# Kernel optimization log

Measured on AMD Instinct MI355X. Metric: run time of the kernel, lower is better.

## Reference

```python
import jax, jax.numpy as jnp
import numpy as np

B = 4096  # batch of 28x28 grayscale images


def setup_inputs() -> dict:
    key = jax.random.key(0)
    k1, k2, k3 = jax.random.split(key, 3)
    x = jax.random.uniform(k1, (B, 28, 28), jnp.float32)
    # 5 trainable rotation angles of the fixed 'RandomLayer' circuit
    rand_params = jax.random.uniform(k2, (5,), jnp.float32, 0.0, 2.0 * np.pi)
    W = jax.random.normal(k3, (10, 4 * 14 * 14), jnp.float32) * 0.02
    b = jnp.zeros((10,), jnp.float32)
    return {"x": x, "rand_params": rand_params, "W": W, "b": b}


def _apply1(state, U, w):
    # state: (N,2,2,2,2) complex; apply 2x2 gate U on wire w
    st = jnp.moveaxis(state, w + 1, -1)
    st = st @ U.T
    return jnp.moveaxis(st, -1, w + 1)


def _apply2(state, U, w1, w2):
    # apply 4x4 gate U on (w1,w2), w1 < w2
    st = jnp.moveaxis(state, (w1 + 1, w2 + 1), (-2, -1))
    shp = st.shape
    st = st.reshape(shp[:-2] + (4,)) @ U.T
    return jnp.moveaxis(st.reshape(shp), (-2, -1), (w1 + 1, w2 + 1))


def _ry(t):
    c = jnp.cos(t / 2).astype(jnp.complex64)
    s = jnp.sin(t / 2).astype(jnp.complex64)
    return jnp.stack([jnp.stack([c, -s]), jnp.stack([s, c])])


def _rx(t):
    c = jnp.cos(t / 2).astype(jnp.complex64)
    s = jnp.sin(t / 2).astype(jnp.complex64)
    return jnp.stack([jnp.stack([c, -1j * s]), jnp.stack([-1j * s, c])])


def _rz(t):
    e = jnp.exp(-0.5j * t).astype(jnp.complex64)
    z = jnp.zeros((), jnp.complex64)
    return jnp.stack([jnp.stack([e, z]), jnp.stack([z, jnp.conj(e)])])


_CNOT = jnp.array([[1, 0, 0, 0], [0, 1, 0, 0], [0, 0, 0, 1], [0, 0, 1, 0]], jnp.complex64)


def _forward(x, rand_params, W, b):
    bsz = x.shape[0]
    # 2x2 patches in row-major (r,c) order; pixel order (r,c),(r,c+1),(r+1,c),(r+1,c+1)
    xp = x.reshape(bsz, 14, 2, 14, 2).transpose(0, 1, 3, 2, 4).reshape(bsz, 196, 4)
    ang = xp.reshape(-1, 4)  # (N,4) angles, N = bsz*196
    c, s = jnp.cos(ang / 2), jnp.sin(ang / 2)
    # Ry(theta_i)|0> on each wire => product state built via einsum
    a = [jnp.stack([c[:, i], s[:, i]], axis=-1) for i in range(4)]
    state = jnp.einsum('na,nb,nc,nd->nabcd', a[0], a[1], a[2], a[3]).astype(jnp.complex64)
    # fixed 8-op 'RandomLayer' circuit
    state = _apply1(state, _ry(rand_params[0]), 0)
    state = _apply1(state, _rx(rand_params[1]), 1)
    state = _apply2(state, _CNOT, 0, 1)
    state = _apply1(state, _rz(rand_params[2]), 2)
    state = _apply1(state, _ry(rand_params[3]), 3)
    state = _apply2(state, _CNOT, 2, 3)
    state = _apply1(state, _rx(rand_params[4]), 0)
    state = _apply2(state, _CNOT, 1, 2)
    # PauliZ expectation per wire
    probs = state.real ** 2 + state.imag ** 2  # (N,2,2,2,2)
    z = jnp.array([1.0, -1.0], jnp.float32)
    ez = [jnp.einsum('nabcd,a->n', probs, z),
          jnp.einsum('nabcd,b->n', probs, z),
          jnp.einsum('nabcd,c->n', probs, z),
          jnp.einsum('nabcd,d->n', probs, z)]
    feats = jnp.stack(ez, axis=-1).reshape(bsz, 196 * 4)
    logits = feats @ W.T + b
    return jax.nn.log_softmax(logits, axis=-1)


def reference(x, rand_params, W, b):
    return _forward(x, rand_params, W, b)
```

## Files before the change

### kernel.cpp

```cpp
#include <hip/hip_runtime.h>
#include <math.h>


#define RY_GATE(bit, c_, s_) do {                                          \
    _Pragma("unroll")                                                      \
    for (int j = 0; j < 8; ++j) {                                          \
        const int lo = ((j >> (bit)) << ((bit) + 1)) | (j & ((1 << (bit)) - 1)); \
        const int hi = lo | (1 << (bit));                                  \
        float u0r = sr[lo], u0i = si[lo], u1r = sr[hi], u1i = si[hi];      \
        sr[lo] = (c_) * u0r - (s_) * u1r; si[lo] = (c_) * u0i - (s_) * u1i; \
        sr[hi] = (s_) * u0r + (c_) * u1r; si[hi] = (s_) * u0i + (c_) * u1i; \
    }                                                                      \
} while (0)

#define RX_GATE(bit, c_, s_) do {                                          \
    _Pragma("unroll")                                                      \
    for (int j = 0; j < 8; ++j) {                                          \
        const int lo = ((j >> (bit)) << ((bit) + 1)) | (j & ((1 << (bit)) - 1)); \
        const int hi = lo | (1 << (bit));                                  \
        float u0r = sr[lo], u0i = si[lo], u1r = sr[hi], u1i = si[hi];      \
        sr[lo] = (c_) * u0r + (s_) * u1i; si[lo] = (c_) * u0i - (s_) * u1r; \
        sr[hi] = (c_) * u1r + (s_) * u0i; si[hi] = (c_) * u1i - (s_) * u0r; \
    }                                                                      \
} while (0)

#define RZ_GATE(bit, c_, s_) do {                                          \
    _Pragma("unroll")                                                      \
    for (int j = 0; j < 8; ++j) {                                          \
        const int lo = ((j >> (bit)) << ((bit) + 1)) | (j & ((1 << (bit)) - 1)); \
        const int hi = lo | (1 << (bit));                                  \
        float r0 = sr[lo], i0 = si[lo], r1 = sr[hi], i1 = si[hi];          \
        sr[lo] = (c_) * r0 + (s_) * i0; si[lo] = (c_) * i0 - (s_) * r0;    \
        sr[hi] = (c_) * r1 - (s_) * i1; si[hi] = (c_) * i1 + (s_) * r1;    \
    }                                                                      \
} while (0)

#define CNOT_GATE(cb, tb) do {                                             \
    _Pragma("unroll")                                                      \
    for (int idx = 0; idx < 16; ++idx) {                                   \
        if (((idx >> (cb)) & 1) && !((idx >> (tb)) & 1)) {                 \
            const int o = idx | (1 << (tb));                               \
            float tr = sr[idx], ti = si[idx];                              \
            sr[idx] = sr[o]; si[idx] = si[o];                              \
            sr[o] = tr;      si[o] = ti;                                   \
        }                                                                  \
    }                                                                      \
} while (0)

__global__ __launch_bounds__(256) void quanv_fused_kernel(
    const float* __restrict__ x,
    const float* __restrict__ rp,
    const float* __restrict__ W,
    const float* __restrict__ bias,
    float* __restrict__ out)
{
    const int img = blockIdx.x;
    const int tid = threadIdx.x;

    float acc[10];
#pragma unroll
    for (int c = 0; c < 10; ++c) acc[c] = 0.0f;

    if (tid < 196) {
        const int pr = tid / 14;
        const int pc = tid - pr * 14;
        const float* px = x + (size_t)img * 784 + (2 * pr) * 28 + 2 * pc;
        const float2 r0 = *(const float2*)(px);
        const float2 r1 = *(const float2*)(px + 28);
        const float ang[4] = { r0.x, r0.y, r1.x, r1.y };

        float ca[4], sa[4];
#pragma unroll
        for (int i = 0; i < 4; ++i) __sincosf(0.5f * ang[i], &sa[i], &ca[i]);

        float sr[16], si[16];
#pragma unroll
        for (int a = 0; a < 2; ++a)
#pragma unroll
            for (int b = 0; b < 2; ++b)
#pragma unroll
                for (int c = 0; c < 2; ++c)
#pragma unroll
                    for (int d = 0; d < 2; ++d) {
                        const int idx = a * 8 + b * 4 + c * 2 + d;
                        sr[idx] = (a ? sa[0] : ca[0]) * (b ? sa[1] : ca[1]) *
                                  (c ? sa[2] : ca[2]) * (d ? sa[3] : ca[3]);
                        si[idx] = 0.0f;
                    }

        float gc[5], gs[5];
#pragma unroll
        for (int i = 0; i < 5; ++i) __sincosf(0.5f * rp[i], &gs[i], &gc[i]);

        RY_GATE(3, gc[0], gs[0]);
        RX_GATE(2, gc[1], gs[1]);
        CNOT_GATE(3, 2);
        RZ_GATE(1, gc[2], gs[2]);
        RY_GATE(0, gc[3], gs[3]);
        CNOT_GATE(1, 0);
        RX_GATE(3, gc[4], gs[4]);
        CNOT_GATE(2, 1);

        float ez0 = 0.f, ez1 = 0.f, ez2 = 0.f, ez3 = 0.f;
#pragma unroll
        for (int idx = 0; idx < 16; ++idx) {
            const float p = sr[idx] * sr[idx] + si[idx] * si[idx];
            ez0 += ((idx >> 3) & 1) ? -p : p;
            ez1 += ((idx >> 2) & 1) ? -p : p;
            ez2 += ((idx >> 1) & 1) ? -p : p;
            ez3 += ((idx >> 0) & 1) ? -p : p;
        }

#pragma unroll
        for (int c = 0; c < 10; ++c) {
            const float4 wv = *(const float4*)(W + c * 784 + tid * 4);
            acc[c] = wv.x * ez0 + wv.y * ez1 + wv.z * ez2 + wv.w * ez3;
        }
    }

#pragma unroll
    for (int c = 0; c < 10; ++c) {
        float v = acc[c];
#pragma unroll
        for (int off = 32; off > 0; off >>= 1) v += __shfl_down(v, off, 64);
        acc[c] = v;
    }

    __shared__ float partial[4][10];
    __shared__ float logits_s[10];
    const int wave = tid >> 6;
    const int lane = tid & 63;
    if (lane == 0) {
#pragma unroll
        for (int c = 0; c < 10; ++c) partial[wave][c] = acc[c];
    }
    __syncthreads();

    if (tid < 10) {
        float l = bias[tid];
#pragma unroll
        for (int w = 0; w < 4; ++w) l += partial[w][tid];
        logits_s[tid] = l;
    }
    __syncthreads();

    if (tid < 10) {
        float m = -INFINITY;
#pragma unroll
        for (int c = 0; c < 10; ++c) m = fmaxf(m, logits_s[c]);
        float sum = 0.0f;
#pragma unroll
        for (int c = 0; c < 10; ++c) sum += __expf(logits_s[c] - m);
        out[(size_t)img * 10 + tid] = logits_s[tid] - m - __logf(sum);
    }
}

extern "C" void kernel_launch(void* const* d_in, const int* in_sizes, int n_in,
                              void* d_out, int out_size, void* d_ws, size_t ws_size,
                              hipStream_t stream) {
    const float* x    = (const float*)d_in[0];
    const float* rp   = (const float*)d_in[1];
    const float* W    = (const float*)d_in[2];
    const float* bias = (const float*)d_in[3];
    float* out = (float*)d_out;

    quanv_fused_kernel<<<4096, 256, 0, stream>>>(x, rp, W, bias, out);
}
```

Baseline: 81.97 us.

## Map one image per wavefront and drop shared-memory block reduction

Each 64-lane wavefront now handles a whole image, looping over its 196 patches in four strided passes, so four images share a 256-thread block and the grid shrinks by a factor of four. The final reduction uses xor shuffles within the wave and computes log-softmax in registers, which removes both __syncthreads and the shared-memory partials. The simulation also skips work on known-zero imaginary parts: the first gates are specialised, and the Z expectations are computed as 1-2*S. In exchange each lane runs a serial loop of four patch simulations, and on the last pass many lanes are idle (196 of 256 slots are used).

New measurement: 78.09 us. 1.05x faster.

```diff
diff --git a/kernel.cpp b/kernel.cpp
--- a/kernel.cpp
+++ b/kernel.cpp
@@ -47,74 +47,107 @@
     }                                                                      \
 } while (0)
 
-__global__ __launch_bounds__(256) void quanv_fused_kernel(
+__device__ __forceinline__ void sim_patch(const float ang[4],
+                                          const float gc[5], const float gs[5],
+                                          float ez[4])
+{
+    float ca[4], sa[4];
+#pragma unroll
+    for (int i = 0; i < 4; ++i) __sincosf(0.5f * ang[i], &sa[i], &ca[i]);
+
+    float ab[4] = { ca[0] * ca[1], ca[0] * sa[1], sa[0] * ca[1], sa[0] * sa[1] };
+    float cd[4] = { ca[2] * ca[3], ca[2] * sa[3], sa[2] * ca[3], sa[2] * sa[3] };
+    float sr[16], si[16];
+#pragma unroll
+    for (int h = 0; h < 4; ++h)
+#pragma unroll
+        for (int l = 0; l < 4; ++l)
+            sr[h * 4 + l] = ab[h] * cd[l];
+
+#pragma unroll
+    for (int j = 0; j < 8; ++j) {
+        const int lo = j, hi = j | 8;
+        float t0 = sr[lo], t1 = sr[hi];
+        sr[lo] = gc[0] * t0 - gs[0] * t1;
+        sr[hi] = gs[0] * t0 + gc[0] * t1;
+    }
+#pragma unroll
+    for (int j = 0; j < 8; ++j) {
+        const int lo = ((j >> 2) << 3) | (j & 3);
+        const int hi = lo | 4;
+        float t0 = sr[lo], t1 = sr[hi];
+        sr[lo] = gc[1] * t0;  si[lo] = -gs[1] * t1;
+        sr[hi] = gc[1] * t1;  si[hi] = -gs[1] * t0;
+    }
+    CNOT_GATE(3, 2);
+    RZ_GATE(1, gc[2], gs[2]);
+    RY_GATE(0, gc[3], gs[3]);
+    CNOT_GATE(1, 0);
+    RX_GATE(3, gc[4], gs[4]);
+    CNOT_GATE(2, 1);
+
+    float p[16];
+#pragma unroll
+    for (int i = 0; i < 16; ++i)
+        p[i] = fmaf(sr[i], sr[i], si[i] * si[i]);
+
+    float S0 = 0.f, S1 = 0.f, S2 = 0.f, S3 = 0.f;
+#pragma unroll
+    for (int i = 0; i < 16; ++i) {
+        if (i & 8) S0 += p[i];
+        if (i & 4) S1 += p[i];
+        if (i & 2) S2 += p[i];
+        if (i & 1) S3 += p[i];
+    }
+    ez[0] = fmaf(-2.f, S0, 1.f);
+    ez[1] = fmaf(-2.f, S1, 1.f);
+    ez[2] = fmaf(-2.f, S2, 1.f);
+    ez[3] = fmaf(-2.f, S3, 1.f);
+}
+
+__global__ __launch_bounds__(256, 4) void quanv_fused_kernel(
     const float* __restrict__ x,
     const float* __restrict__ rp,
     const float* __restrict__ W,
     const float* __restrict__ bias,
     float* __restrict__ out)
 {
-    const int img = blockIdx.x;
-    const int tid = threadIdx.x;
+    const int tid  = threadIdx.x;
+    const int lane = tid & 63;
+    const int img  = (blockIdx.x << 2) + (tid >> 6);
+
+    float gc[5], gs[5];
+#pragma unroll
+    for (int i = 0; i < 5; ++i) __sincosf(0.5f * rp[i], &gs[i], &gc[i]);
 
     float acc[10];
 #pragma unroll
     for (int c = 0; c < 10; ++c) acc[c] = 0.0f;
 
-    if (tid < 196) {
-        const int pr = tid / 14;
-        const int pc = tid - pr * 14;
-        const float* px = x + (size_t)img * 784 + (2 * pr) * 28 + 2 * pc;
-        const float2 r0 = *(const float2*)(px);
-        const float2 r1 = *(const float2*)(px + 28);
-        const float ang[4] = { r0.x, r0.y, r1.x, r1.y };
+    const float* xb = x + (size_t)img * 784;
 
-        float ca[4], sa[4];
-#pragma unroll
-        for (int i = 0; i < 4; ++i) __sincosf(0.5f * ang[i], &sa[i], &ca[i]);
+#pragma unroll 1
+    for (int k = 0; k < 4; ++k) {
+        const int pidx = lane + (k << 6);
+        if (pidx < 196) {
+            const int pr = pidx / 14;
+            const int pc = pidx - pr * 14;
+            const float* px = xb + pr * 56 + pc * 2;
+            const float2 r0 = *(const float2*)(px);
+            const float2 r1 = *(const float2*)(px + 28);
+            const float ang[4] = { r0.x, r0.y, r1.x, r1.y };
 
-        float sr[16], si[16];
-#pragma unroll
-        for (int a = 0; a < 2; ++a)
-#pragma unroll
-            for (int b = 0; b < 2; ++b)
-#pragma unroll
-                for (int c = 0; c < 2; ++c)
-#pragma unroll
-                    for (int d = 0; d < 2; ++d) {
-                        const int idx = a * 8 + b * 4 + c * 2 + d;
-                        sr[idx] = (a ? sa[0] : ca[0]) * (b ? sa[1] : ca[1]) *
-                                  (c ? sa[2] : ca[2]) * (d ? sa[3] : ca[3]);
-                        si[idx] = 0.0f;
-                    }
-
-        float gc[5], gs[5];
-#pragma unroll
-        for (int i = 0; i < 5; ++i) __sincosf(0.5f * rp[i], &gs[i], &gc[i]);
-
-        RY_GATE(3, gc[0], gs[0]);
-        RX_GATE(2, gc[1], gs[1]);
-        CNOT_GATE(3, 2);
-        RZ_GATE(1, gc[2], gs[2]);
-        RY_GATE(0, gc[3], gs[3]);
-        CNOT_GATE(1, 0);
-        RX_GATE(3, gc[4], gs[4]);
-        CNOT_GATE(2, 1);
-
-        float ez0 = 0.f, ez1 = 0.f, ez2 = 0.f, ez3 = 0.f;
-#pragma unroll
-        for (int idx = 0; idx < 16; ++idx) {
-            const float p = sr[idx] * sr[idx] + si[idx] * si[idx];
-            ez0 += ((idx >> 3) & 1) ? -p : p;
-            ez1 += ((idx >> 2) & 1) ? -p : p;
-            ez2 += ((idx >> 1) & 1) ? -p : p;
-            ez3 += ((idx >> 0) & 1) ? -p : p;
-        }
+            float ez[4];
+            sim_patch(ang, gc, gs, ez);
 
 #pragma unroll
-        for (int c = 0; c < 10; ++c) {
-            const float4 wv = *(const float4*)(W + c * 784 + tid * 4);
-            acc[c] = wv.x * ez0 + wv.y * ez1 + wv.z * ez2 + wv.w * ez3;
+            for (int c = 0; c < 10; ++c) {
+                const float4 wv = *(const float4*)(W + c * 784 + pidx * 4);
+                acc[c] = fmaf(wv.x, ez[0],
+                         fmaf(wv.y, ez[1],
+                         fmaf(wv.z, ez[2],
+                         fmaf(wv.w, ez[3], acc[c]))));
+            }
         }
     }
 
@@ -122,37 +155,22 @@
     for (int c = 0; c < 10; ++c) {
         float v = acc[c];
 #pragma unroll
-        for (int off = 32; off > 0; off >>= 1) v += __shfl_down(v, off, 64);
-        acc[c] = v;
+        for (int off = 32; off > 0; off >>= 1) v += __shfl_xor(v, off, 64);
+        acc[c] = v + bias[c];
     }
 
-    __shared__ float partial[4][10];
-    __shared__ float logits_s[10];
-    const int wave = tid >> 6;
-    const int lane = tid & 63;
-    if (lane == 0) {
+    float m = acc[0];
 #pragma unroll
-        for (int c = 0; c < 10; ++c) partial[wave][c] = acc[c];
-    }
-    __syncthreads();
+    for (int c = 1; c < 10; ++c) m = fmaxf(m, acc[c]);
+    float s = 0.0f;
+#pragma unroll
+    for (int c = 0; c < 10; ++c) s += __expf(acc[c] - m);
+    const float lse = m + __logf(s);
 
-    if (tid < 10) {
-        float l = bias[tid];
+    float myv = acc[0];
 #pragma unroll
-        for (int w = 0; w < 4; ++w) l += partial[w][tid];
-        logits_s[tid] = l;
-    }
-    __syncthreads();
-
-    if (tid < 10) {
-        float m = -INFINITY;
-#pragma unroll
-        for (int c = 0; c < 10; ++c) m = fmaxf(m, logits_s[c]);
-        float sum = 0.0f;
-#pragma unroll
-        for (int c = 0; c < 10; ++c) sum += __expf(logits_s[c] - m);
-        out[(size_t)img * 10 + tid] = logits_s[tid] - m - __logf(sum);
-    }
+    for (int c = 1; c < 10; ++c) myv = (lane == c) ? acc[c] : myv;
+    if (lane < 10) out[(size_t)img * 10 + lane] = myv - lse;
 }
 
 extern "C" void kernel_launch(void* const* d_in, const int* in_sizes, int n_in,
@@ -164,5 +182,5 @@
     const float* bias = (const float*)d_in[3];
     float* out = (float*)d_out;
 
-    quanv_fused_kernel<<<4096, 256, 0, stream>>>(x, rp, W, bias, out);
+    quanv_fused_kernel<<<1024, 256, 0, stream>>>(x, rp, W, bias, out);
 }
```
